# Performance work log

Hardware: AMD Instinct MI355X
Metric: run time of the kernel (lower is better)

The kernel has to match this reference:

```python
import jax, jax.numpy as jnp
import numpy as np
from jax import lax

B, T, V, L = 256, 512, 256, 64
EPS = 1e-7  # keras backend epsilon used by ctc_batch_cost
NEG = -1e30  # log(0) surrogate, safe in float32


def setup_inputs() -> dict:
    key = jax.random.key(0)
    k1, k2 = jax.random.split(key)
    # labels in [0, V-1): class V-1 is reserved for the CTC blank
    y_true = jax.random.randint(k1, (B, L), 0, V - 1)
    # ctc_batch_cost expects probabilities (softmax output)
    logits = jax.random.normal(k2, (B, T, V), dtype=jnp.float32)
    y_pred = jax.nn.softmax(logits, axis=-1)
    return {"y_true": y_true, "y_pred": y_pred}


def reference(y_true, y_pred):
    """Keras ctc_batch_cost: per-example CTC negative log-likelihood, shape [B,1].

    Matches TF semantics: blank = V-1, log(y_pred + eps), full input/label lengths,
    merge-repeated forward DP in log space.
    """
    b, t, v = y_pred.shape
    l = y_true.shape[1]
    S = 2 * l + 1  # extended label: blank-interleaved
    blank = v - 1

    logp = jnp.log(y_pred + EPS)  # [B,T,V]

    # extended label sequence z: blank at even positions, labels at odd
    ext = jnp.full((b, S), blank, dtype=y_true.dtype).at[:, 1::2].set(y_true)  # [B,S]

    # lp[b,t,s] = logp[b,t,ext[b,s]]
    idx = jnp.broadcast_to(ext[:, None, :], (b, t, S))
    lp = jnp.take_along_axis(logp, idx, axis=2)  # [B,T,S]

    # skip transition s-2 -> s allowed iff z[s] != blank and z[s] != z[s-2]
    ext_m2 = jnp.concatenate([jnp.full((b, 2), -1, dtype=ext.dtype), ext[:, :-2]], axis=1)
    skip = (ext != blank) & (ext != ext_m2)  # [B,S]

    # alpha at t=0: only first blank or first label reachable
    alpha0 = jnp.full((b, S), NEG, dtype=logp.dtype)
    alpha0 = alpha0.at[:, 0].set(lp[:, 0, 0]).at[:, 1].set(lp[:, 0, 1])

    neg1 = jnp.full((b, 1), NEG, dtype=logp.dtype)
    neg2 = jnp.full((b, 2), NEG, dtype=logp.dtype)

    def step(alpha, lpt):
        a1 = jnp.concatenate([neg1, alpha[:, :-1]], axis=1)
        a2 = jnp.concatenate([neg2, alpha[:, :-2]], axis=1)
        m = jnp.logaddexp(alpha, a1)
        m = jnp.where(skip, jnp.logaddexp(m, a2), m)
        return m + lpt, None

    lp_t = jnp.moveaxis(lp[:, 1:], 1, 0)  # [T-1, B, S] time-major
    alphaT, _ = lax.scan(step, alpha0, lp_t)

    loss = -jnp.logaddexp(alphaT[:, -1], alphaT[:, -2])  # [B]
    return loss[:, None]
```

## Files before the change

kernel.cpp:

```cpp
#include <hip/hip_runtime.h>
#include <math.h>


#define BB   256
#define TI   512
#define VV   256
#define LL   64
#define TT   16
#define NT   (TI / TT)
#define EPSF 1e-7f
#define NEGF -1e30f
#define LN2F 0.6931471805599453f

#if __has_builtin(__builtin_amdgcn_exp2f)
__device__ __forceinline__ float fexp2(float x) { return __builtin_amdgcn_exp2f(x); }
#else
__device__ __forceinline__ float fexp2(float x) { return __exp2f(x); }
#endif
#if __has_builtin(__builtin_amdgcn_logf)
__device__ __forceinline__ float flog2(float x) { return __builtin_amdgcn_logf(x); }
#else
__device__ __forceinline__ float flog2(float x) { return __log2f(x); }
#endif

__device__ __forceinline__ float shup_neg(float x) {
    int r = __builtin_amdgcn_update_dpp(__float_as_int(NEGF), __float_as_int(x),
                                        0x138 , 0xF, 0xF, false);
    return __int_as_float(r);
}

__device__ __forceinline__ float lae2(float a, float b) {
    float m = fmaxf(a, b);
    float d = fminf(a, b) - m;
    return m + flog2(1.0f + fexp2(d));
}
__device__ __forceinline__ float lae3(float a, float b, float c) {
    float m = fmaxf(fmaxf(a, b), c);
    float s = fexp2(a - m) + fexp2(b - m) + fexp2(c - m);
    return m + flog2(s);
}

__device__ __forceinline__ void dp_step(float& a0, float& a1, float& a128,
                                        float lpb, float lpl, bool skip) {
    float pa1  = shup_neg(a1);
    float pa1s = skip ? pa1 : NEGF;
    float na0   = lae2(a0, pa1) + lpb;
    float na1   = lae3(a1, a0, pa1s) + lpl;
    float na128 = lae2(a128, a1) + lpb;
    a0 = na0; a1 = na1; a128 = na128;
}

__device__ __forceinline__ void stage_tile(const float* gsrc, float* lbase, int lane) {
    #pragma unroll
    for (int i = 0; i < TT; ++i) {
        __builtin_amdgcn_global_load_lds(
            (const __attribute__((address_space(1))) void*)(gsrc + i * VV + lane * 4),
            (__attribute__((address_space(3))) void*)(lbase + i * VV),
            16, 0, 0);
    }
}

__device__ __forceinline__ void prep_lp(const float* sb, int myLab,
                                        float (&lpb)[TT], float (&lpl)[TT]) {
    #pragma unroll
    for (int tt = 0; tt < TT; ++tt) {
        float xb = sb[tt * VV + (VV - 1)];
        float xl = sb[tt * VV + myLab];
        lpb[tt] = flog2(xb + EPSF);
        lpl[tt] = flog2(xl + EPSF);
    }
}

__global__ __launch_bounds__(64) void ctc_kernel(
        const int* __restrict__ y_true,
        const float* __restrict__ y_pred,
        float* __restrict__ out) {
    __shared__ float sbuf[3 * TT * VV];

    const int b    = blockIdx.x;
    const int lane = threadIdx.x;
    const float* src = y_pred + (size_t)b * TI * VV;

    const int myLab = y_true[b * LL + lane];
    const int prevLab = __shfl_up(myLab, 1);
    const bool skip = (lane == 0) ? true : (myLab != prevLab);

    stage_tile(src,               sbuf,               lane);
    stage_tile(src + TT * VV,     sbuf + TT * VV,     lane);
    asm volatile("s_waitcnt vmcnt(16)" ::: "memory");

    float clpb[TT], clpl[TT], nlpb[TT], nlpl[TT];
    prep_lp(sbuf, myLab, clpb, clpl);

    float a0   = (lane == 0) ? clpb[0] : NEGF;
    float a1   = (lane == 0) ? clpl[0] : NEGF;
    float a128 = NEGF;

    for (int k = 0; k < NT; ++k) {
        if (k + 2 < NT)
            stage_tile(src + (size_t)(k + 2) * TT * VV,
                       sbuf + ((k + 2) % 3) * TT * VV, lane);

        if (k + 1 < NT) {
            if (k + 2 < NT) asm volatile("s_waitcnt vmcnt(16)" ::: "memory");
            else            asm volatile("s_waitcnt vmcnt(0)"  ::: "memory");
            prep_lp(sbuf + ((k + 1) % 3) * TT * VV, myLab, nlpb, nlpl);
        }

        if (k == 0) {
            #pragma unroll
            for (int tt = 1; tt < TT; ++tt)
                dp_step(a0, a1, a128, clpb[tt], clpl[tt], skip);
        } else {
            #pragma unroll
            for (int tt = 0; tt < TT; ++tt)
                dp_step(a0, a1, a128, clpb[tt], clpl[tt], skip);
        }

        if (k + 1 < NT) {
            #pragma unroll
            for (int tt = 0; tt < TT; ++tt) { clpb[tt] = nlpb[tt]; clpl[tt] = nlpl[tt]; }
        }
    }

    if (lane == 63) out[b] = -(lae2(a128, a1) * LN2F);
}

extern "C" void kernel_launch(void* const* d_in, const int* in_sizes, int n_in,
                              void* d_out, int out_size, void* d_ws, size_t ws_size,
                              hipStream_t stream) {
    const int*   y_true = (const int*)d_in[0];
    const float* y_pred = (const float*)d_in[1];
    float*       out    = (float*)d_out;
    ctc_kernel<<<dim3(BB), dim3(64), 0, stream>>>(y_true, y_pred, out);
}
```

Baseline: 202.9 us.

## Run CTC forward DP in scaled probability space instead of log space

Replaces the log-space recurrence (a max, an exp2 and a log2 per logaddexp) with linear-space products and sums of probabilities. Every 8 timesteps the alphas are renormalised by the wave-wide maximum, found with a DPP reduction, and the log of that scale is accumulated. This removes the transcendental ops and the per-element log of the inputs from the serial dependency chain. The cost is a periodic cross-lane reduction, plus a risk of underflow or precision loss between rescales.

```diff
diff --git a/kernel.cpp b/kernel.cpp
--- a/kernel.cpp
+++ b/kernel.cpp
@@ -9,44 +9,49 @@
 #define TT   16
 #define NT   (TI / TT)
 #define EPSF 1e-7f
-#define NEGF -1e30f
 #define LN2F 0.6931471805599453f
 
-#if __has_builtin(__builtin_amdgcn_exp2f)
-__device__ __forceinline__ float fexp2(float x) { return __builtin_amdgcn_exp2f(x); }
-#else
-__device__ __forceinline__ float fexp2(float x) { return __exp2f(x); }
-#endif
 #if __has_builtin(__builtin_amdgcn_logf)
 __device__ __forceinline__ float flog2(float x) { return __builtin_amdgcn_logf(x); }
 #else
 __device__ __forceinline__ float flog2(float x) { return __log2f(x); }
 #endif
 
-__device__ __forceinline__ float shup_neg(float x) {
-    int r = __builtin_amdgcn_update_dpp(__float_as_int(NEGF), __float_as_int(x),
-                                        0x138 , 0xF, 0xF, false);
-    return __int_as_float(r);
+template <int CTRL>
+__device__ __forceinline__ float dppf(float oldv, float v) {
+    return __int_as_float(__builtin_amdgcn_update_dpp(
+        __float_as_int(oldv), __float_as_int(v), CTRL, 0xF, 0xF, false));
 }
 
-__device__ __forceinline__ float lae2(float a, float b) {
-    float m = fmaxf(a, b);
-    float d = fminf(a, b) - m;
-    return m + flog2(1.0f + fexp2(d));
+__device__ __forceinline__ float shup0(float x) { return dppf<0x138>(0.0f, x); }
+
+__device__ __forceinline__ float wave_max_bcast(float v) {
+    v = fmaxf(v, dppf<0x111>(v, v));
+    v = fmaxf(v, dppf<0x112>(v, v));
+    v = fmaxf(v, dppf<0x114>(v, v));
+    v = fmaxf(v, dppf<0x118>(v, v));
+    v = fmaxf(v, dppf<0x142>(v, v));
+    v = fmaxf(v, dppf<0x143>(v, v));
+    return __int_as_float(__builtin_amdgcn_readlane(__float_as_int(v), 63));
 }
-__device__ __forceinline__ float lae3(float a, float b, float c) {
-    float m = fmaxf(fmaxf(a, b), c);
-    float s = fexp2(a - m) + fexp2(b - m) + fexp2(c - m);
-    return m + flog2(s);
+
+__device__ __forceinline__ void rescale(float& a0, float& a1, float& a128,
+                                        float& logC) {
+    float m = wave_max_bcast(fmaxf(fmaxf(a0, a1), a128));
+    m = fmaxf(m, 1e-37f);
+    float s = __builtin_amdgcn_rcpf(m);
+    a0 *= s; a1 *= s; a128 *= s;
+    logC += flog2(m);
 }
 
 __device__ __forceinline__ void dp_step(float& a0, float& a1, float& a128,
-                                        float lpb, float lpl, bool skip) {
-    float pa1  = shup_neg(a1);
-    float pa1s = skip ? pa1 : NEGF;
-    float na0   = lae2(a0, pa1) + lpb;
-    float na1   = lae3(a1, a0, pa1s) + lpl;
-    float na128 = lae2(a128, a1) + lpb;
+                                        float pb, float pl, float skipf) {
+    float pa1 = shup0(a1);
+    float s01 = a0 + a1;
+    float t0  = a0 + pa1;
+    float na1   = fmaf(pa1, skipf, s01) * pl;
+    float na0   = t0 * pb;
+    float na128 = (a128 + a1) * pb;
     a0 = na0; a1 = na1; a128 = na128;
 }
 
@@ -60,14 +65,12 @@
     }
 }
 
-__device__ __forceinline__ void prep_lp(const float* sb, int myLab,
-                                        float (&lpb)[TT], float (&lpl)[TT]) {
+__device__ __forceinline__ void prep_p(const float* sb, int myLab,
+                                       float (&pb)[TT], float (&pl)[TT]) {
     #pragma unroll
     for (int tt = 0; tt < TT; ++tt) {
-        float xb = sb[tt * VV + (VV - 1)];
-        float xl = sb[tt * VV + myLab];
-        lpb[tt] = flog2(xb + EPSF);
-        lpl[tt] = flog2(xl + EPSF);
+        pb[tt] = sb[tt * VV + (VV - 1)] + EPSF;
+        pl[tt] = sb[tt * VV + myLab]    + EPSF;
     }
 }
 
@@ -81,20 +84,21 @@
     const int lane = threadIdx.x;
     const float* src = y_pred + (size_t)b * TI * VV;
 
-    const int myLab = y_true[b * LL + lane];
+    const int myLab   = y_true[b * LL + lane];
     const int prevLab = __shfl_up(myLab, 1);
-    const bool skip = (lane == 0) ? true : (myLab != prevLab);
+    const float skipf = (lane == 0 || myLab != prevLab) ? 1.0f : 0.0f;
 
-    stage_tile(src,               sbuf,               lane);
-    stage_tile(src + TT * VV,     sbuf + TT * VV,     lane);
+    stage_tile(src,           sbuf,           lane);
+    stage_tile(src + TT * VV, sbuf + TT * VV, lane);
     asm volatile("s_waitcnt vmcnt(16)" ::: "memory");
 
-    float clpb[TT], clpl[TT], nlpb[TT], nlpl[TT];
-    prep_lp(sbuf, myLab, clpb, clpl);
+    float cpb[TT], cpl[TT], npb[TT], npl[TT];
+    prep_p(sbuf, myLab, cpb, cpl);
 
-    float a0   = (lane == 0) ? clpb[0] : NEGF;
-    float a1   = (lane == 0) ? clpl[0] : NEGF;
-    float a128 = NEGF;
+    float a0   = (lane == 0) ? cpb[0] : 0.0f;
+    float a1   = (lane == 0) ? cpl[0] : 0.0f;
+    float a128 = 0.0f;
+    float logC = 0.0f;
 
     for (int k = 0; k < NT; ++k) {
         if (k + 2 < NT)
@@ -104,26 +108,27 @@
         if (k + 1 < NT) {
             if (k + 2 < NT) asm volatile("s_waitcnt vmcnt(16)" ::: "memory");
             else            asm volatile("s_waitcnt vmcnt(0)"  ::: "memory");
-            prep_lp(sbuf + ((k + 1) % 3) * TT * VV, myLab, nlpb, nlpl);
+            prep_p(sbuf + ((k + 1) % 3) * TT * VV, myLab, npb, npl);
         }
 
-        if (k == 0) {
-            #pragma unroll
-            for (int tt = 1; tt < TT; ++tt)
-                dp_step(a0, a1, a128, clpb[tt], clpl[tt], skip);
-        } else {
-            #pragma unroll
-            for (int tt = 0; tt < TT; ++tt)
-                dp_step(a0, a1, a128, clpb[tt], clpl[tt], skip);
+        #pragma unroll
+        for (int tt = 0; tt < TT; ++tt) {
+            if (!(k == 0 && tt == 0))
+                dp_step(a0, a1, a128, cpb[tt], cpl[tt], skipf);
+            if ((tt & 7) == 7)
+                rescale(a0, a1, a128, logC);
         }
 
         if (k + 1 < NT) {
             #pragma unroll
-            for (int tt = 0; tt < TT; ++tt) { clpb[tt] = nlpb[tt]; clpl[tt] = nlpl[tt]; }
+            for (int tt = 0; tt < TT; ++tt) { cpb[tt] = npb[tt]; cpl[tt] = npl[tt]; }
         }
     }
 
-    if (lane == 63) out[b] = -(lae2(a128, a1) * LN2F);
+    if (lane == 63) {
+        float tail = fmaxf(a128 + a1, 1e-37f);
+        out[b] = -LN2F * (logC + flog2(tail));
+    }
 }
 
 extern "C" void kernel_launch(void* const* d_in, const int* in_sizes, int n_in,
```

Measured after the change: 193.9 us. 1.05x faster.
